# Performance work log

Measured on AMD Instinct MI355X. Metric: run time of the kernel, lower is better.

## Reference

```python
import jax, jax.numpy as jnp
import numpy as np

B, N, NS, D, H = 32, 4096, 16, 512, 8
DH = D // H          # dims_per_head = 64
DFF = 4 * D          # ff_mlp hidden
SCALE = DH ** -0.5
EPS = 1e-8           # slot-attention renorm eps
LN_EPS = 1e-5        # torch LayerNorm default
ITERS = 3


def layer_norm(x, g, b):
    mu = jnp.mean(x, axis=-1, keepdims=True)
    var = jnp.mean((x - mu) ** 2, axis=-1, keepdims=True)
    return (x - mu) * jax.lax.rsqrt(var + LN_EPS) * g + b


def setup_inputs() -> dict:
    key = jax.random.key(0)
    ks = jax.random.split(key, 8)
    s = 0.02
    return {
        "inputs": jax.random.normal(ks[0], (B, N, D), jnp.float32),
        "conditioning": jax.random.normal(ks[1], (B, NS, D), jnp.float32),
        # norm_input
        "ln_in_g": jnp.ones((D,), jnp.float32),
        "ln_in_b": jnp.zeros((D,), jnp.float32),
        # projections (no bias: use_projection_bias=False)
        "Wk": jax.random.normal(ks[2], (D, D), jnp.float32) * s,
        "Wv": jax.random.normal(ks[3], (D, D), jnp.float32) * s,
        "Wq": jax.random.normal(ks[4], (D, D), jnp.float32) * s,
        "Wo": jax.random.normal(ks[5], (D, D), jnp.float32) * s,
        # norm_slots / norm_slots_ff_mlp
        "ln_s_g": jnp.ones((D,), jnp.float32),
        "ln_s_b": jnp.zeros((D,), jnp.float32),
        "ln_f_g": jnp.ones((D,), jnp.float32),
        "ln_f_b": jnp.zeros((D,), jnp.float32),
        # ff_mlp: Linear(D,4D) -> ReLU -> Linear(4D,D)
        "W1": jax.random.normal(ks[6], (D, DFF), jnp.float32) * s,
        "b1": jnp.zeros((DFF,), jnp.float32),
        "W2": jax.random.normal(ks[7], (DFF, D), jnp.float32) * s,
        "b2": jnp.zeros((D,), jnp.float32),
    }


def reference(inputs, conditioning, ln_in_g, ln_in_b, Wk, Wv, Wq, Wo,
              ln_s_g, ln_s_b, ln_f_g, ln_f_b, W1, b1, W2, b2):
    b = inputs.shape[0]
    x = layer_norm(inputs, ln_in_g, ln_in_b)                 # [b, n, D]
    k = (x @ Wk.T).reshape(b, N, H, DH)                      # [b, n, h, dh]
    v = (x @ Wv.T).reshape(b, N, H, DH)

    slots = conditioning
    attn_mean = None
    for _ in range(ITERS):
        slots_prev = slots
        s = layer_norm(slots, ln_s_g, ln_s_b)
        q = (s @ Wq.T).reshape(b, NS, H, DH)                 # [b, ns, h, dh]
        dots = jnp.einsum("bihd,bjhd->bihj", q, k) * SCALE   # [b, ns, h, n]
        # softmax over flattened (slots, heads) axis, per input location j
        attn = jax.nn.softmax(dots.reshape(b, NS * H, N), axis=1)
        attn = attn.reshape(b, NS, H, N)
        attn_before = attn
        attn = attn + EPS
        attn = attn / jnp.sum(attn, axis=-1, keepdims=True)  # renorm over j
        updates = jnp.einsum("bjhd,bihj->bihd", v, attn)     # [b, ns, h, dh]
        updates = updates.reshape(b, NS, D)
        slots = updates @ Wo.T + slots_prev                  # to_o + residual
        slots_prev_ff = slots
        s2 = layer_norm(slots, ln_f_g, ln_f_b)
        s2 = jax.nn.relu(s2 @ W1 + b1) @ W2 + b2             # ff_mlp
        slots = s2 + slots_prev_ff
        attn_mean = jnp.mean(attn_before, axis=2)            # [b, ns, n]
    return slots, attn_mean
```

## Files before the change

kernel.cpp:

```cpp
#include <hip/hip_runtime.h>
#include <cstdint>
#include <cstddef>

typedef __attribute__((ext_vector_type(8))) short short8;
typedef __attribute__((ext_vector_type(4))) short short4v;
typedef __attribute__((ext_vector_type(8))) __bf16 bf16x8;
typedef __attribute__((ext_vector_type(4))) float f32x4;
typedef unsigned short u16;

static constexpr int Bb = 32, Nn = 4096, NSs = 16, Dd = 512, Hh = 8, DFF = 2048;
static constexpr float SCALE = 0.125f;
static constexpr float EPSR  = 1e-8f;
static constexpr float LN_EPS = 1e-5f;
static constexpr int JS = 16;

__device__ __forceinline__ u16 f2b(float x) {
  union { float f; uint32_t u; } a; a.f = x;
  uint32_t r = a.u + 0x7fffu + ((a.u >> 16) & 1u);
  return (u16)(r >> 16);
}
__device__ __forceinline__ float b2f(u16 x) {
  union { uint32_t u; float f; } a; a.u = ((uint32_t)x) << 16; return a.f;
}

__device__ __forceinline__ f32x4 mfma16(short8 a, short8 b, f32x4 c) {
  return __builtin_amdgcn_mfma_f32_16x16x32_bf16(
      __builtin_bit_cast(bf16x8, a), __builtin_bit_cast(bf16x8, b), c, 0, 0, 0);
}

__device__ __forceinline__ void gload16(const u16* g, u16* l) {
  __builtin_amdgcn_global_load_lds(
      (const __attribute__((address_space(1))) void*)g,
      (__attribute__((address_space(3))) void*)l, 16, 0, 0);
}

__global__ __launch_bounds__(256) void ln_rows(const float* __restrict__ src,
    const float* __restrict__ g, const float* __restrict__ bt,
    u16* __restrict__ dst, int R) {
  int row = blockIdx.x * 4 + (threadIdx.x >> 6);
  if (row >= R) return;
  int lane = threadIdx.x & 63;
  const float* p = src + (size_t)row * Dd + lane * 8;
  float4 u0 = *(const float4*)p;
  float4 u1 = *(const float4*)(p + 4);
  float x[8] = {u0.x,u0.y,u0.z,u0.w,u1.x,u1.y,u1.z,u1.w};
  float s = 0.f, s2 = 0.f;
#pragma unroll
  for (int e = 0; e < 8; ++e) { s += x[e]; s2 += x[e]*x[e]; }
#pragma unroll
  for (int m = 1; m < 64; m <<= 1) { s += __shfl_xor(s, m); s2 += __shfl_xor(s2, m); }
  float mean = s * (1.f/512.f);
  float var  = s2 * (1.f/512.f) - mean*mean;
  float rstd = rsqrtf(var + LN_EPS);
  union { u16 o[8]; short8 v; } ou;
#pragma unroll
  for (int e = 0; e < 8; ++e)
    ou.o[e] = f2b((x[e]-mean)*rstd*g[lane*8+e] + bt[lane*8+e]);
  *(short8*)(dst + (size_t)row * Dd + lane * 8) = ou.v;
}

__global__ __launch_bounds__(512, 2) void gemm_kv(const u16* __restrict__ A,
    const u16* __restrict__ Bk, const u16* __restrict__ Bv,
    u16* __restrict__ Ck, u16* __restrict__ CvT) {
  __shared__ u16 lA[2][256*64];
  __shared__ u16 lK[2][128*64];
  __shared__ u16 lV[2][128*64];
  const int tid = threadIdx.x, lane = tid & 63, wid = tid >> 6;
  const int wr = wid >> 2, wn = wid & 3;
  const int n = blockIdx.x;
  const int orig = (n & 7) * 256 + (n >> 3);
  const int bm = (orig >> 2) * 256, bn = (orig & 3) * 128;
  const size_t BN = (size_t)Bb * Nn;
  f32x4 ak[8][2] = {};
  f32x4 av[8][2] = {};
  const int sr = lane >> 3;
  const int ss = ((lane & 7) ^ (sr & 7)) * 8;
  const int li = lane & 15, lk = lane >> 4;
#define STG_A(buf, tt, h) do { \
    gload16(A + (size_t)(bm + (h)*128 + wid*16 + sr) * Dd + (tt)*64 + ss, \
            &lA[buf][((h)*128 + wid*16) * 64]); \
    gload16(A + (size_t)(bm + (h)*128 + wid*16 + 8 + sr) * Dd + (tt)*64 + ss, \
            &lA[buf][((h)*128 + wid*16 + 8) * 64]); \
  } while (0)
#define STG_K(buf, tt) do { \
    gload16(Bk + (size_t)(bn + wid*16 + sr) * Dd + (tt)*64 + ss, \
            &lK[buf][(wid*16) * 64]); \
    gload16(Bk + (size_t)(bn + wid*16 + 8 + sr) * Dd + (tt)*64 + ss, \
            &lK[buf][(wid*16 + 8) * 64]); \
  } while (0)
#define STG_V(buf, tt) do { \
    gload16(Bv + (size_t)(bn + wid*16 + sr) * Dd + (tt)*64 + ss, \
            &lV[buf][(wid*16) * 64]); \
    gload16(Bv + (size_t)(bn + wid*16 + 8 + sr) * Dd + (tt)*64 + ss, \
            &lV[buf][(wid*16 + 8) * 64]); \
  } while (0)
#define PH_ENTER() do { \
    __builtin_amdgcn_sched_barrier(0); \
    __builtin_amdgcn_s_barrier(); \
    asm volatile("s_waitcnt lgkmcnt(0)" ::: "memory"); \
    __builtin_amdgcn_sched_barrier(0); \
    __builtin_amdgcn_s_setprio(1); \
  } while (0)
#define PH_EXIT() do { \
    __builtin_amdgcn_s_setprio(0); \
    __builtin_amdgcn_sched_barrier(0); \
    __builtin_amdgcn_s_barrier(); \
    __builtin_amdgcn_sched_barrier(0); \
  } while (0)
#define PH_EXIT_VM(nvm) do { \
    __builtin_amdgcn_s_setprio(0); \
    __builtin_amdgcn_sched_barrier(0); \
    if (nvm) asm volatile("s_waitcnt vmcnt(2)" ::: "memory"); \
    else     asm volatile("s_waitcnt vmcnt(0)" ::: "memory"); \
    __builtin_amdgcn_sched_barrier(0); \
    __builtin_amdgcn_s_barrier(); \
    __builtin_amdgcn_sched_barrier(0); \
  } while (0)
  STG_A(0, 0, 0);
  STG_A(0, 0, 1);
  STG_K(0, 0);
  STG_V(0, 0);
  asm volatile("s_waitcnt vmcnt(2)" ::: "memory");
  __builtin_amdgcn_sched_barrier(0);
  __builtin_amdgcn_s_barrier();
  __builtin_amdgcn_sched_barrier(0);
  for (int t = 0; t < 8; ++t) {
    const int cb = t & 1, nb = cb ^ 1, tn = t + 1;
    const bool nl = (t != 7);
    short8 afA[4][2], afB[4][2], kf[2][2], vf[2][2];
#pragma unroll
    for (int m = 0; m < 4; ++m)
#pragma unroll
      for (int ks = 0; ks < 2; ++ks)
        afA[m][ks] = *(const short8*)&lA[cb][(wr*128 + m*16 + li)*64
                                            + (((ks*4 + lk) ^ (li & 7))*8)];
#pragma unroll
    for (int c = 0; c < 2; ++c)
#pragma unroll
      for (int ks = 0; ks < 2; ++ks)
        kf[c][ks] = *(const short8*)&lK[cb][(wn*32 + c*16 + li)*64
                                            + (((ks*4 + lk) ^ (li & 7))*8)];
    if (nl) STG_A(nb, tn, 0);
    PH_ENTER();
#pragma unroll
    for (int m = 0; m < 4; ++m)
#pragma unroll
      for (int c = 0; c < 2; ++c)
#pragma unroll
        for (int ks = 0; ks < 2; ++ks)
          ak[m][c] = mfma16(kf[c][ks], afA[m][ks], ak[m][c]);
    PH_EXIT_VM(nl);
#pragma unroll
    for (int c = 0; c < 2; ++c)
#pragma unroll
      for (int ks = 0; ks < 2; ++ks)
        vf[c][ks] = *(const short8*)&lV[cb][(wn*32 + c*16 + li)*64
                                            + (((ks*4 + lk) ^ (li & 7))*8)];
    if (nl) STG_A(nb, tn, 1);
    PH_ENTER();
#pragma unroll
    for (int m = 0; m < 4; ++m)
#pragma unroll
      for (int c = 0; c < 2; ++c)
#pragma unroll
        for (int ks = 0; ks < 2; ++ks)
          av[m][c] = mfma16(afA[m][ks], vf[c][ks], av[m][c]);
    PH_EXIT();
#pragma unroll
    for (int m = 0; m < 4; ++m)
#pragma unroll
      for (int ks = 0; ks < 2; ++ks)
        afB[m][ks] = *(const short8*)&lA[cb][(wr*128 + (m + 4)*16 + li)*64
                                            + (((ks*4 + lk) ^ (li & 7))*8)];
    if (nl) STG_K(nb, tn);
    PH_ENTER();
#pragma unroll
    for (int m = 0; m < 4; ++m)
#pragma unroll
      for (int c = 0; c < 2; ++c)
#pragma unroll
        for (int ks = 0; ks < 2; ++ks)
          ak[m + 4][c] = mfma16(kf[c][ks], afB[m][ks], ak[m + 4][c]);
    PH_EXIT();
    if (nl) STG_V(nb, tn);
    PH_ENTER();
#pragma unroll
    for (int m = 0; m < 4; ++m)
#pragma unroll
      for (int c = 0; c < 2; ++c)
#pragma unroll
        for (int ks = 0; ks < 2; ++ks)
          av[m + 4][c] = mfma16(afB[m][ks], vf[c][ks], av[m + 4][c]);
    PH_EXIT_VM(nl);
  }
#undef STG_A
#undef STG_K
#undef STG_V
#undef PH_ENTER
#undef PH_EXIT
#undef PH_EXIT_VM
#pragma unroll
  for (int m = 0; m < 8; ++m)
#pragma unroll
    for (int c = 0; c < 2; ++c) {
      {
        int row = bm + wr*128 + m*16 + li;
        int c0  = bn + wn*32 + c*16 + lk*4;
        f32x4 vk = ak[m][c];
        union { u16 o[4]; short4v v4; } ou;
#pragma unroll
        for (int r = 0; r < 4; ++r) ou.o[r] = f2b(vk[r]);
        *(short4v*)&Ck[(size_t)row * Dd + c0] = ou.v4;
      }
      {
        int col = bn + wn*32 + c*16 + li;
        int r0  = bm + wr*128 + m*16 + lk*4;
        f32x4 vv = av[m][c];
        union { u16 o[4]; short4v v4; } ou;
#pragma unroll
        for (int r = 0; r < 4; ++r) ou.o[r] = f2b(vv[r]);
        *(short4v*)&CvT[(size_t)col * BN + r0] = ou.v4;
      }
    }
}

template<int EP>
__global__ __launch_bounds__(256) void gemm64(const u16* __restrict__ A,
    const u16* __restrict__ Bw, void* __restrict__ Cp,
    const float* __restrict__ bias, const float* __restrict__ res,
    int N, int K) {
  const int lane = threadIdx.x & 63, wid = threadIdx.x >> 6;
  const int wr = wid >> 1, wc = wid & 1;
  const int bm = blockIdx.y * 64, bn = blockIdx.x * 64;
  const int li = lane & 15, lk = lane >> 4;
  f32x4 acc[2][2] = {};
  const u16* Ap = A  + (size_t)(bm + wr*32 + li) * K + lk*8;
  const u16* Bp = Bw + (size_t)(bn + wc*32 + li) * K + lk*8;
#pragma unroll 4
  for (int k0 = 0; k0 < K; k0 += 32) {
    short8 af[2], bf[2];
    af[0] = *(const short8*)(Ap + k0);
    af[1] = *(const short8*)(Ap + (size_t)16*K + k0);
    bf[0] = *(const short8*)(Bp + k0);
    bf[1] = *(const short8*)(Bp + (size_t)16*K + k0);
#pragma unroll
    for (int m = 0; m < 2; ++m)
#pragma unroll
      for (int nn2 = 0; nn2 < 2; ++nn2)
        acc[m][nn2] = mfma16(bf[nn2], af[m], acc[m][nn2]);
  }
#pragma unroll
  for (int m = 0; m < 2; ++m)
#pragma unroll
    for (int nn2 = 0; nn2 < 2; ++nn2) {
      int row = bm + wr*32 + m*16 + li;
      int c0  = bn + wc*32 + nn2*16 + lk*4;
      size_t off = (size_t)row * N + c0;
      f32x4 v = acc[m][nn2];
      if constexpr (EP == 0) {
        union { u16 o[4]; short4v v4; } ou;
#pragma unroll
        for (int r = 0; r < 4; ++r) ou.o[r] = f2b(v[r]);
        *(short4v*)&((u16*)Cp)[off] = ou.v4;
      } else if constexpr (EP == 1) {
        float4 rr = *(const float4*)&res[off];
        float4 o = {v[0] + rr.x, v[1] + rr.y, v[2] + rr.z, v[3] + rr.w};
        *(float4*)&((float*)Cp)[off] = o;
      } else if constexpr (EP == 2) {
        float4 bb = *(const float4*)&bias[c0];
        union { u16 o[4]; short4v v4; } ou;
        float x0 = v[0] + bb.x, x1 = v[1] + bb.y, x2 = v[2] + bb.z, x3 = v[3] + bb.w;
        ou.o[0] = f2b(x0 > 0.f ? x0 : 0.f); ou.o[1] = f2b(x1 > 0.f ? x1 : 0.f);
        ou.o[2] = f2b(x2 > 0.f ? x2 : 0.f); ou.o[3] = f2b(x3 > 0.f ? x3 : 0.f);
        *(short4v*)&((u16*)Cp)[off] = ou.v4;
      } else {
        float4 bb = *(const float4*)&bias[c0];
        float4 rr = *(const float4*)&res[off];
        float4 o = {v[0] + bb.x + rr.x, v[1] + bb.y + rr.y,
                    v[2] + bb.z + rr.z, v[3] + bb.w + rr.w};
        *(float4*)&((float*)Cp)[off] = o;
      }
    }
}

__global__ __launch_bounds__(512, 4) void attn_f(const u16* __restrict__ q,
    const u16* __restrict__ kk, const u16* __restrict__ vT,
    float* __restrict__ rowsum, float* __restrict__ Tpart,
    float* __restrict__ attn_mean) {
  const int js = blockIdx.x, b = blockIdx.y;
  const int tid = threadIdx.x, lane = tid & 63, h = tid >> 6;
  __shared__ float redM[8][64];
  __shared__ float redS[8][64];
  __shared__ u16 P2[8][16][72];
  const int li = lane & 15, lk = lane >> 4;
  const size_t BN = (size_t)Bb * Nn;
  const u16* qb = q + (((size_t)b*16 + li)*8 + h)*64 + lk*8;
  short8 a0 = *(const short8*)qb;
  short8 a1 = *(const short8*)(qb + 32);
  f32x4 apv[4] = {};
  float rs_acc[4] = {0.f, 0.f, 0.f, 0.f};
  for (int t2 = 0; t2 < 4; ++t2) {
    const int j0 = js * 256 + t2 * 64;
    f32x4 dt[4];
#pragma unroll
    for (int n = 0; n < 4; ++n) {
      const u16* kb = kk + ((size_t)b*Nn + j0 + n*16 + li)*Dd + h*64 + lk*8;
      f32x4 acc = {};
      acc = mfma16(a0, *(const short8*)kb, acc);
      acc = mfma16(a1, *(const short8*)(kb + 32), acc);
#pragma unroll
      for (int r = 0; r < 4; ++r) dt[n][r] = acc[r] * SCALE;
    }
#pragma unroll
    for (int n = 0; n < 4; ++n) {
      float v = fmaxf(fmaxf(dt[n][0], dt[n][1]), fmaxf(dt[n][2], dt[n][3]));
      v = fmaxf(v, __shfl_xor(v, 16));
      v = fmaxf(v, __shfl_xor(v, 32));
      if (lk == 0) redM[h][n*16 + li] = v;
    }
    __syncthreads();
    float M[4];
#pragma unroll
    for (int n = 0; n < 4; ++n) {
      float m2 = redM[0][n*16 + li];
#pragma unroll
      for (int p = 1; p < 8; ++p) m2 = fmaxf(m2, redM[p][n*16 + li]);
      M[n] = m2;
    }
#pragma unroll
    for (int n = 0; n < 4; ++n) {
      float s = 0.f;
#pragma unroll
      for (int r = 0; r < 4; ++r) { dt[n][r] = __expf(dt[n][r] - M[n]); s += dt[n][r]; }
      s += __shfl_xor(s, 16);
      s += __shfl_xor(s, 32);
      if (lk == 0) redS[h][n*16 + li] = s;
    }
    __syncthreads();
#pragma unroll
    for (int n = 0; n < 4; ++n) {
      float s2 = redS[0][n*16 + li];
#pragma unroll
      for (int p = 1; p < 8; ++p) s2 += redS[p][n*16 + li];
      float inv = 1.f / s2;
#pragma unroll
      for (int r = 0; r < 4; ++r) dt[n][r] = dt[n][r] * inv + EPSR;
    }
#pragma unroll
    for (int n = 0; n < 4; ++n)
#pragma unroll
      for (int r = 0; r < 4; ++r)
        P2[h][lk*4 + r][n*16 + li] = f2b(dt[n][r]);
#pragma unroll
    for (int r = 0; r < 4; ++r) {
      float v = dt[0][r] + dt[1][r] + dt[2][r] + dt[3][r];
      v += __shfl_xor(v, 1); v += __shfl_xor(v, 2);
      v += __shfl_xor(v, 4); v += __shfl_xor(v, 8);
      rs_acc[r] += v;
    }
    short8 pa0 = *(const short8*)&P2[h][li][lk*8];
    short8 pa1 = *(const short8*)&P2[h][li][32 + lk*8];
#pragma unroll
    for (int n = 0; n < 4; ++n) {
      const u16* vb = vT + (size_t)(h*64 + n*16 + li)*BN + (size_t)b*Nn + j0 + lk*8;
      apv[n] = mfma16(*(const short8*)vb, pa0, apv[n]);
      apv[n] = mfma16(*(const short8*)(vb + 32), pa1, apv[n]);
    }
    if (attn_mean != nullptr) {
      __syncthreads();
      int j = tid & 63;
#pragma unroll
      for (int ii = 0; ii < 2; ++ii) {
        int i = (tid >> 6) + ii*8;
        float sm = 0.f;
#pragma unroll
        for (int hh = 0; hh < 8; ++hh) sm += b2f(P2[hh][i][j]);
        attn_mean[((size_t)b*16 + i)*Nn + j0 + j] = sm * 0.125f - EPSR;
      }
      __syncthreads();
    }
  }
  float* Tout = Tpart + (((size_t)js * Bb + b) * 8 + h) * 16 * 64;
#pragma unroll
  for (int n = 0; n < 4; ++n) {
    float4 o = {apv[n][0], apv[n][1], apv[n][2], apv[n][3]};
    *(float4*)&Tout[(size_t)li * 64 + n*16 + lk*4] = o;
  }
  if (li == 0)
#pragma unroll
    for (int r = 0; r < 4; ++r)
      atomicAdd(&rowsum[b*128 + (lk*4 + r)*8 + h], rs_acc[r]);
}

__global__ void upd_c(const float* __restrict__ Tpart,
    const float* __restrict__ rs, u16* __restrict__ updb) {
  int idx = blockIdx.x * 256 + threadIdx.x;
  int o = idx & 511, bi = idx >> 9;
  int b = bi >> 4, i = bi & 15;
  int h = o >> 6, d = o & 63;
  size_t base = (((size_t)b * 8 + h) * 16 + i) * 64 + d;
  const size_t stride = (size_t)Bb * 8 * 16 * 64;
  float t = 0.f;
#pragma unroll
  for (int p = 0; p < JS; ++p) t += Tpart[base + p * stride];
  updb[idx] = f2b(t / rs[b * 128 + i * 8 + h]);
}

__global__ void cvt_w(const float* __restrict__ s, u16* __restrict__ d, int n) {
  int i = blockIdx.x*256 + threadIdx.x;
  if (i < n) d[i] = f2b(s[i]);
}
__global__ __launch_bounds__(256) void tr_cvt(const float* __restrict__ s,
    u16* __restrict__ d, int R, int C) {
  __shared__ u16 t[32][33];
  const int c0 = blockIdx.x*32, r0 = blockIdx.y*32;
  const int tr = threadIdx.x >> 3, tc4 = (threadIdx.x & 7)*4;
  float4 v = *(const float4*)&s[(size_t)(r0+tr)*C + c0 + tc4];
  t[tr][tc4+0] = f2b(v.x); t[tr][tc4+1] = f2b(v.y);
  t[tr][tc4+2] = f2b(v.z); t[tr][tc4+3] = f2b(v.w);
  __syncthreads();
  const int oc = threadIdx.x >> 3, or4 = (threadIdx.x & 7)*4;
  union { u16 o[4]; short4v v4; } ou;
#pragma unroll
  for (int e = 0; e < 4; ++e) ou.o[e] = t[or4+e][oc];
  *(short4v*)&d[(size_t)(c0+oc)*R + r0 + or4] = ou.v4;
}
__global__ void copy_f32v4(const float* __restrict__ s, float* __restrict__ d, int n4) {
  int i = blockIdx.x*256 + threadIdx.x;
  if (i < n4) ((float4*)d)[i] = ((const float4*)s)[i];
}

extern "C" void kernel_launch(void* const* d_in, const int* in_sizes, int n_in,
                              void* d_out, int out_size, void* d_ws, size_t ws_size,
                              hipStream_t stream) {
  (void)in_sizes; (void)n_in; (void)out_size; (void)ws_size;
  const float* inputs  = (const float*)d_in[0];
  const float* cond    = (const float*)d_in[1];
  const float* ln_in_g = (const float*)d_in[2];
  const float* ln_in_b = (const float*)d_in[3];
  const float* Wk = (const float*)d_in[4];
  const float* Wv = (const float*)d_in[5];
  const float* Wq = (const float*)d_in[6];
  const float* Wo = (const float*)d_in[7];
  const float* ln_s_g = (const float*)d_in[8];
  const float* ln_s_b = (const float*)d_in[9];
  const float* ln_f_g = (const float*)d_in[10];
  const float* ln_f_b = (const float*)d_in[11];
  const float* W1 = (const float*)d_in[12];
  const float* b1 = (const float*)d_in[13];
  const float* W2 = (const float*)d_in[14];
  const float* b2 = (const float*)d_in[15];
  float* out_slots = (float*)d_out;
  float* out_amean = (float*)d_out + (size_t)Bb*NSs*Dd;

  char* w = (char*)d_ws;
  auto alloc = [&](size_t bytes) {
    char* p = w; w += (bytes + 255) & ~(size_t)255; return p;
  };
  u16*  xn    = (u16*)alloc((size_t)Bb*Nn*Dd*2);
  u16*  kbuf  = (u16*)alloc((size_t)Bb*Nn*Dd*2);
  u16*  vT    = (u16*)alloc((size_t)Bb*Nn*Dd*2);
  float* Tpart = (float*)alloc((size_t)JS*Bb*8*16*64*4);
  float* slots = (float*)alloc((size_t)Bb*NSs*Dd*4);
  u16*  qb    = (u16*)alloc((size_t)Bb*NSs*Dd*2);
  u16*  snb   = (u16*)alloc((size_t)Bb*NSs*Dd*2);
  u16*  s2nb  = (u16*)alloc((size_t)Bb*NSs*Dd*2);
  u16*  h1b   = (u16*)alloc((size_t)Bb*NSs*DFF*2);
  u16*  updb  = (u16*)alloc((size_t)Bb*NSs*Dd*2);
  float* rowsum = (float*)alloc((size_t)Bb*128*3*4);
  u16*  wkb = (u16*)alloc(262144*2);
  u16*  wvb = (u16*)alloc(262144*2);
  u16*  wqb = (u16*)alloc(262144*2);
  u16*  wob = (u16*)alloc(262144*2);
  u16*  w1t = (u16*)alloc((size_t)1048576*2);
  u16*  w2t = (u16*)alloc((size_t)1048576*2);

  cvt_w<<<1024, 256, 0, stream>>>(Wk, wkb, 262144);
  cvt_w<<<1024, 256, 0, stream>>>(Wv, wvb, 262144);
  cvt_w<<<1024, 256, 0, stream>>>(Wq, wqb, 262144);
  cvt_w<<<1024, 256, 0, stream>>>(Wo, wob, 262144);
  tr_cvt<<<dim3(64, 16), 256, 0, stream>>>(W1, w1t, 512, 2048);
  tr_cvt<<<dim3(16, 64), 256, 0, stream>>>(W2, w2t, 2048, 512);
  copy_f32v4<<<256, 256, 0, stream>>>(cond, slots, 65536);
  (void)hipMemsetAsync(rowsum, 0, (size_t)Bb*128*3*4, stream);
  ln_rows<<<Bb*Nn/4, 256, 0, stream>>>(inputs, ln_in_g, ln_in_b, xn, Bb*Nn);
  gemm_kv<<<2048, 512, 0, stream>>>(xn, wkb, wvb, kbuf, vT);

  for (int it = 0; it < 3; ++it) {
    float* rsp = rowsum + (size_t)it * Bb * 128;
    ln_rows<<<128, 256, 0, stream>>>(slots, ln_s_g, ln_s_b, snb, Bb*NSs);
    gemm64<0><<<dim3(8, 8), 256, 0, stream>>>(snb, wqb, qb, nullptr, nullptr, 512, 512);
    attn_f<<<dim3(JS, Bb), 512, 0, stream>>>(qb, kbuf, vT, rsp, Tpart,
                                             it == 2 ? out_amean : nullptr);
    upd_c<<<1024, 256, 0, stream>>>(Tpart, rsp, updb);
    gemm64<1><<<dim3(8, 8), 256, 0, stream>>>(updb, wob, slots, nullptr, slots, 512, 512);
    ln_rows<<<128, 256, 0, stream>>>(slots, ln_f_g, ln_f_b, s2nb, Bb*NSs);
    gemm64<2><<<dim3(32, 8), 256, 0, stream>>>(s2nb, w1t, h1b, b1, nullptr, 2048, 512);
    gemm64<3><<<dim3(8, 8), 256, 0, stream>>>(h1b, w2t, slots, b2, slots, 512, 2048);
  }
  copy_f32v4<<<256, 256, 0, stream>>>(slots, out_slots, 65536);
}
```

Before: 700.3 us.

## Fuse slot LayerNorms and partial-sum combine into the small GEMM prologues

```diff
diff --git a/kernel.cpp b/kernel.cpp
--- a/kernel.cpp
+++ b/kernel.cpp
@@ -225,8 +225,135 @@
 }
 
 template<int EP>
-__global__ __launch_bounds__(256) void gemm64(const u16* __restrict__ A,
+__device__ __forceinline__ void gemm_from_lds(const u16* lAbase,
     const u16* __restrict__ Bw, void* __restrict__ Cp,
+    const float* __restrict__ bias, const float* __restrict__ res,
+    int bm, int bn, int N) {
+  const int lane = threadIdx.x & 63, wid = threadIdx.x >> 6;
+  const int wr = wid >> 1, wc = wid & 1;
+  const int li = lane & 15, lk = lane >> 4;
+  f32x4 acc[2][2] = {};
+  const u16* Bp = Bw + (size_t)(bn + wc*32 + li) * Dd + lk*8;
+#pragma unroll 4
+  for (int k0 = 0; k0 < Dd; k0 += 32) {
+    short8 af[2], bf[2];
+#pragma unroll
+    for (int m = 0; m < 2; ++m) {
+      int row = wr*32 + m*16 + li;
+      af[m] = *(const short8*)&lAbase[row*512 + (((k0 >> 3) + lk) ^ (row & 7))*8];
+    }
+    bf[0] = *(const short8*)(Bp + k0);
+    bf[1] = *(const short8*)(Bp + (size_t)16*Dd + k0);
+#pragma unroll
+    for (int m = 0; m < 2; ++m)
+#pragma unroll
+      for (int nn2 = 0; nn2 < 2; ++nn2)
+        acc[m][nn2] = mfma16(bf[nn2], af[m], acc[m][nn2]);
+  }
+#pragma unroll
+  for (int m = 0; m < 2; ++m)
+#pragma unroll
+    for (int nn2 = 0; nn2 < 2; ++nn2) {
+      int row = bm + wr*32 + m*16 + li;
+      int c0  = bn + wc*32 + nn2*16 + lk*4;
+      size_t off = (size_t)row * N + c0;
+      f32x4 v = acc[m][nn2];
+      if constexpr (EP == 0) {
+        union { u16 o[4]; short4v v4; } ou;
+#pragma unroll
+        for (int r = 0; r < 4; ++r) ou.o[r] = f2b(v[r]);
+        *(short4v*)&((u16*)Cp)[off] = ou.v4;
+      } else if constexpr (EP == 1) {
+        float4 rr = *(const float4*)&res[off];
+        float4 o = {v[0] + rr.x, v[1] + rr.y, v[2] + rr.z, v[3] + rr.w};
+        *(float4*)&((float*)Cp)[off] = o;
+      } else if constexpr (EP == 2) {
+        float4 bb = *(const float4*)&bias[c0];
+        union { u16 o[4]; short4v v4; } ou;
+        float x0 = v[0] + bb.x, x1 = v[1] + bb.y, x2 = v[2] + bb.z, x3 = v[3] + bb.w;
+        ou.o[0] = f2b(x0 > 0.f ? x0 : 0.f); ou.o[1] = f2b(x1 > 0.f ? x1 : 0.f);
+        ou.o[2] = f2b(x2 > 0.f ? x2 : 0.f); ou.o[3] = f2b(x3 > 0.f ? x3 : 0.f);
+        *(short4v*)&((u16*)Cp)[off] = ou.v4;
+      }
+    }
+}
+
+template<int EP>
+__global__ __launch_bounds__(256) void lngemm(const float* __restrict__ src,
+    const float* __restrict__ g, const float* __restrict__ bt,
+    const u16* __restrict__ Bw, void* __restrict__ Cp,
+    const float* __restrict__ bias, int N) {
+  __shared__ u16 lA[64 * 512];
+  const int tid = threadIdx.x;
+  const int bm = blockIdx.y * 64, bn = blockIdx.x * 64;
+  {
+    const int r = tid >> 2, q4 = tid & 3;
+    const float* p = src + (size_t)(bm + r) * Dd + q4 * 128;
+    float s = 0.f, s2 = 0.f;
+#pragma unroll
+    for (int c4 = 0; c4 < 32; ++c4) {
+      float4 v = *(const float4*)(p + c4 * 4);
+      s += v.x + v.y + v.z + v.w;
+      s2 += v.x*v.x + v.y*v.y + v.z*v.z + v.w*v.w;
+    }
+    s += __shfl_xor(s, 1); s2 += __shfl_xor(s2, 1);
+    s += __shfl_xor(s, 2); s2 += __shfl_xor(s2, 2);
+    float mean = s * (1.f/512.f);
+    float var  = s2 * (1.f/512.f) - mean*mean;
+    float rstd = rsqrtf(var + LN_EPS);
+#pragma unroll
+    for (int e = 0; e < 16; ++e) {
+      int k = q4 * 128 + e * 8;
+      union { u16 o[8]; short8 v; } ou;
+#pragma unroll
+      for (int j = 0; j < 8; ++j)
+        ou.o[j] = f2b((p[e*8 + j - 0] - mean) * rstd * g[k + j] + bt[k + j]);
+      int slot = (k >> 3) ^ (r & 7);
+      *(short8*)&lA[r * 512 + slot * 8] = ou.v;
+    }
+  }
+  __syncthreads();
+  gemm_from_lds<EP>(lA, Bw, Cp, bias, nullptr, bm, bn, N);
+}
+
+__global__ __launch_bounds__(256) void cmbgemm(const float* __restrict__ Tpart,
+    const float* __restrict__ rs, const u16* __restrict__ Bw,
+    float* __restrict__ Cp, const float* __restrict__ res) {
+  __shared__ u16 lA[64 * 512];
+  const int tid = threadIdx.x;
+  const int bm = blockIdx.y * 64, bn = blockIdx.x * 64;
+  {
+    const int r = tid >> 2, q4 = tid & 3;
+    const int bi = bm + r, b = bi >> 4, i = bi & 15;
+    const size_t stride = (size_t)Bb * 8 * 16 * 64;
+#pragma unroll
+    for (int e = 0; e < 16; ++e) {
+      int c = q4 * 128 + e * 8;
+      int h = c >> 6, d = c & 63;
+      size_t base = (((size_t)b * 8 + h) * 16 + i) * 64 + d;
+      float4 a0 = {0.f,0.f,0.f,0.f}, a1 = {0.f,0.f,0.f,0.f};
+      for (int p = 0; p < JS; ++p) {
+        float4 v0 = *(const float4*)&Tpart[base + p * stride];
+        float4 v1 = *(const float4*)&Tpart[base + p * stride + 4];
+        a0.x += v0.x; a0.y += v0.y; a0.z += v0.z; a0.w += v0.w;
+        a1.x += v1.x; a1.y += v1.y; a1.z += v1.z; a1.w += v1.w;
+      }
+      float inv = 1.f / rs[b * 128 + i * 8 + h];
+      union { u16 o[8]; short8 v; } ou;
+      ou.o[0] = f2b(a0.x*inv); ou.o[1] = f2b(a0.y*inv);
+      ou.o[2] = f2b(a0.z*inv); ou.o[3] = f2b(a0.w*inv);
+      ou.o[4] = f2b(a1.x*inv); ou.o[5] = f2b(a1.y*inv);
+      ou.o[6] = f2b(a1.z*inv); ou.o[7] = f2b(a1.w*inv);
+      int slot = (c >> 3) ^ (r & 7);
+      *(short8*)&lA[r * 512 + slot * 8] = ou.v;
+    }
+  }
+  __syncthreads();
+  gemm_from_lds<1>(lA, Bw, Cp, nullptr, res, bm, bn, 512);
+}
+
+__global__ __launch_bounds__(256) void gemm64_ep3(const u16* __restrict__ A,
+    const u16* __restrict__ Bw, float* __restrict__ Cp,
     const float* __restrict__ bias, const float* __restrict__ res,
     int N, int K) {
   const int lane = threadIdx.x & 63, wid = threadIdx.x >> 6;
@@ -257,29 +384,11 @@
       int c0  = bn + wc*32 + nn2*16 + lk*4;
       size_t off = (size_t)row * N + c0;
       f32x4 v = acc[m][nn2];
-      if constexpr (EP == 0) {
-        union { u16 o[4]; short4v v4; } ou;
-#pragma unroll
-        for (int r = 0; r < 4; ++r) ou.o[r] = f2b(v[r]);
-        *(short4v*)&((u16*)Cp)[off] = ou.v4;
-      } else if constexpr (EP == 1) {
-        float4 rr = *(const float4*)&res[off];
-        float4 o = {v[0] + rr.x, v[1] + rr.y, v[2] + rr.z, v[3] + rr.w};
-        *(float4*)&((float*)Cp)[off] = o;
-      } else if constexpr (EP == 2) {
-        float4 bb = *(const float4*)&bias[c0];
-        union { u16 o[4]; short4v v4; } ou;
-        float x0 = v[0] + bb.x, x1 = v[1] + bb.y, x2 = v[2] + bb.z, x3 = v[3] + bb.w;
-        ou.o[0] = f2b(x0 > 0.f ? x0 : 0.f); ou.o[1] = f2b(x1 > 0.f ? x1 : 0.f);
-        ou.o[2] = f2b(x2 > 0.f ? x2 : 0.f); ou.o[3] = f2b(x3 > 0.f ? x3 : 0.f);
-        *(short4v*)&((u16*)Cp)[off] = ou.v4;
-      } else {
-        float4 bb = *(const float4*)&bias[c0];
-        float4 rr = *(const float4*)&res[off];
-        float4 o = {v[0] + bb.x + rr.x, v[1] + bb.y + rr.y,
-                    v[2] + bb.z + rr.z, v[3] + bb.w + rr.w};
-        *(float4*)&((float*)Cp)[off] = o;
-      }
+      float4 bb = *(const float4*)&bias[c0];
+      float4 rr = *(const float4*)&res[off];
+      float4 o = {v[0] + bb.x + rr.x, v[1] + bb.y + rr.y,
+                  v[2] + bb.z + rr.z, v[3] + bb.w + rr.w};
+      *(float4*)&Cp[off] = o;
     }
 }
 
@@ -390,20 +499,6 @@
 #pragma unroll
     for (int r = 0; r < 4; ++r)
       atomicAdd(&rowsum[b*128 + (lk*4 + r)*8 + h], rs_acc[r]);
-}
-
-__global__ void upd_c(const float* __restrict__ Tpart,
-    const float* __restrict__ rs, u16* __restrict__ updb) {
-  int idx = blockIdx.x * 256 + threadIdx.x;
-  int o = idx & 511, bi = idx >> 9;
-  int b = bi >> 4, i = bi & 15;
-  int h = o >> 6, d = o & 63;
-  size_t base = (((size_t)b * 8 + h) * 16 + i) * 64 + d;
-  const size_t stride = (size_t)Bb * 8 * 16 * 64;
-  float t = 0.f;
-#pragma unroll
-  for (int p = 0; p < JS; ++p) t += Tpart[base + p * stride];
-  updb[idx] = f2b(t / rs[b * 128 + i * 8 + h]);
 }
 
 __global__ void cvt_w(const float* __restrict__ s, u16* __restrict__ d, int n) {
@@ -463,10 +558,7 @@
   float* Tpart = (float*)alloc((size_t)JS*Bb*8*16*64*4);
   float* slots = (float*)alloc((size_t)Bb*NSs*Dd*4);
   u16*  qb    = (u16*)alloc((size_t)Bb*NSs*Dd*2);
-  u16*  snb   = (u16*)alloc((size_t)Bb*NSs*Dd*2);
-  u16*  s2nb  = (u16*)alloc((size_t)Bb*NSs*Dd*2);
   u16*  h1b   = (u16*)alloc((size_t)Bb*NSs*DFF*2);
-  u16*  updb  = (u16*)alloc((size_t)Bb*NSs*Dd*2);
   float* rowsum = (float*)alloc((size_t)Bb*128*3*4);
   u16*  wkb = (u16*)alloc(262144*2);
   u16*  wvb = (u16*)alloc(262144*2);
@@ -488,15 +580,15 @@
 
   for (int it = 0; it < 3; ++it) {
     float* rsp = rowsum + (size_t)it * Bb * 128;
-    ln_rows<<<128, 256, 0, stream>>>(slots, ln_s_g, ln_s_b, snb, Bb*NSs);
-    gemm64<0><<<dim3(8, 8), 256, 0, stream>>>(snb, wqb, qb, nullptr, nullptr, 512, 512);
+    lngemm<0><<<dim3(8, 8), 256, 0, stream>>>(slots, ln_s_g, ln_s_b, wqb, qb,
+                                              nullptr, 512);
     attn_f<<<dim3(JS, Bb), 512, 0, stream>>>(qb, kbuf, vT, rsp, Tpart,
                                              it == 2 ? out_amean : nullptr);
-    upd_c<<<1024, 256, 0, stream>>>(Tpart, rsp, updb);
-    gemm64<1><<<dim3(8, 8), 256, 0, stream>>>(updb, wob, slots, nullptr, slots, 512, 512);
-    ln_rows<<<128, 256, 0, stream>>>(slots, ln_f_g, ln_f_b, s2nb, Bb*NSs);
-    gemm64<2><<<dim3(32, 8), 256, 0, stream>>>(s2nb, w1t, h1b, b1, nullptr, 2048, 512);
-    gemm64<3><<<dim3(8, 8), 256, 0, stream>>>(h1b, w2t, slots, b2, slots, 512, 2048);
+    cmbgemm<<<dim3(8, 8), 256, 0, stream>>>(Tpart, rsp, wob, slots, slots);
+    lngemm<2><<<dim3(32, 8), 256, 0, stream>>>(slots, ln_f_g, ln_f_b, w1t, h1b,
+                                               b1, 2048);
+    gemm64_ep3<<<dim3(8, 8), 256, 0, stream>>>(h1b, w2t, slots, b2, slots,
+                                               512, 2048);
   }
   copy_f32v4<<<256, 256, 0, stream>>>(slots, out_slots, 65536);
 }
```

New measurement: 1.007 ms. 43.7% more time.

## Fuse slot LayerNorm and Q projection into attention kernel

Applied to the files above, without the earlier changes.

```diff
diff --git a/kernel.cpp b/kernel.cpp
--- a/kernel.cpp
+++ b/kernel.cpp
@@ -257,12 +257,7 @@
       int c0  = bn + wc*32 + nn2*16 + lk*4;
       size_t off = (size_t)row * N + c0;
       f32x4 v = acc[m][nn2];
-      if constexpr (EP == 0) {
-        union { u16 o[4]; short4v v4; } ou;
-#pragma unroll
-        for (int r = 0; r < 4; ++r) ou.o[r] = f2b(v[r]);
-        *(short4v*)&((u16*)Cp)[off] = ou.v4;
-      } else if constexpr (EP == 1) {
+      if constexpr (EP == 1) {
         float4 rr = *(const float4*)&res[off];
         float4 o = {v[0] + rr.x, v[1] + rr.y, v[2] + rr.z, v[3] + rr.w};
         *(float4*)&((float*)Cp)[off] = o;
@@ -283,20 +278,69 @@
     }
 }
 
-__global__ __launch_bounds__(512, 4) void attn_f(const u16* __restrict__ q,
-    const u16* __restrict__ kk, const u16* __restrict__ vT,
-    float* __restrict__ rowsum, float* __restrict__ Tpart,
-    float* __restrict__ attn_mean) {
+__global__ __launch_bounds__(512, 4) void attn_f(const float* __restrict__ slots,
+    const float* __restrict__ lng, const float* __restrict__ lnb,
+    const u16* __restrict__ Wq, const u16* __restrict__ kk,
+    const u16* __restrict__ vT, float* __restrict__ rowsum,
+    float* __restrict__ Tpart, float* __restrict__ attn_mean) {
   const int js = blockIdx.x, b = blockIdx.y;
   const int tid = threadIdx.x, lane = tid & 63, h = tid >> 6;
   __shared__ float redM[8][64];
   __shared__ float redS[8][64];
   __shared__ u16 P2[8][16][72];
+  __shared__ u16 ls[16 * 520];
+  __shared__ u16 lq[16 * 520];
   const int li = lane & 15, lk = lane >> 4;
   const size_t BN = (size_t)Bb * Nn;
-  const u16* qb = q + (((size_t)b*16 + li)*8 + h)*64 + lk*8;
-  short8 a0 = *(const short8*)qb;
-  short8 a1 = *(const short8*)(qb + 32);
+  {
+    const int r = 2*h + (lane >> 5);
+    const int c0 = (lane & 31) * 16;
+    const float* p = slots + ((size_t)b*16 + r) * Dd + c0;
+    float4 v0 = *(const float4*)p;
+    float4 v1 = *(const float4*)(p + 4);
+    float4 v2 = *(const float4*)(p + 8);
+    float4 v3 = *(const float4*)(p + 12);
+    float x[16] = {v0.x,v0.y,v0.z,v0.w, v1.x,v1.y,v1.z,v1.w,
+                   v2.x,v2.y,v2.z,v2.w, v3.x,v3.y,v3.z,v3.w};
+    float s = 0.f, s2 = 0.f;
+#pragma unroll
+    for (int e = 0; e < 16; ++e) { s += x[e]; s2 += x[e]*x[e]; }
+#pragma unroll
+    for (int m = 1; m < 32; m <<= 1) { s += __shfl_xor(s, m); s2 += __shfl_xor(s2, m); }
+    float mean = s * (1.f/512.f);
+    float var  = s2 * (1.f/512.f) - mean*mean;
+    float rstd = rsqrtf(var + LN_EPS);
+    union { u16 o[8]; short8 v; } oa, ob;
+#pragma unroll
+    for (int e = 0; e < 8; ++e) {
+      oa.o[e] = f2b((x[e]   - mean) * rstd * lng[c0 + e]     + lnb[c0 + e]);
+      ob.o[e] = f2b((x[e+8] - mean) * rstd * lng[c0 + 8 + e] + lnb[c0 + 8 + e]);
+    }
+    *(short8*)&ls[r * 520 + c0] = oa.v;
+    *(short8*)&ls[r * 520 + c0 + 8] = ob.v;
+  }
+  __syncthreads();
+  {
+    f32x4 qacc[4] = {};
+    const u16* Wp = Wq + (size_t)(h*64 + li) * Dd + lk*8;
+#pragma unroll 4
+    for (int k0 = 0; k0 < 512; k0 += 32) {
+      short8 af = *(const short8*)&ls[li*520 + k0 + lk*8];
+#pragma unroll
+      for (int n = 0; n < 4; ++n) {
+        short8 bf = *(const short8*)(Wp + (size_t)(n*16)*Dd + k0);
+        qacc[n] = mfma16(af, bf, qacc[n]);
+      }
+    }
+#pragma unroll
+    for (int n = 0; n < 4; ++n)
+#pragma unroll
+      for (int r = 0; r < 4; ++r)
+        lq[(lk*4 + r)*520 + h*64 + n*16 + li] = f2b(qacc[n][r]);
+  }
+  __syncthreads();
+  short8 a0 = *(const short8*)&lq[li*520 + h*64 + lk*8];
+  short8 a1 = *(const short8*)&lq[li*520 + h*64 + 32 + lk*8];
   f32x4 apv[4] = {};
   float rs_acc[4] = {0.f, 0.f, 0.f, 0.f};
   for (int t2 = 0; t2 < 4; ++t2) {
@@ -462,8 +506,6 @@
   u16*  vT    = (u16*)alloc((size_t)Bb*Nn*Dd*2);
   float* Tpart = (float*)alloc((size_t)JS*Bb*8*16*64*4);
   float* slots = (float*)alloc((size_t)Bb*NSs*Dd*4);
-  u16*  qb    = (u16*)alloc((size_t)Bb*NSs*Dd*2);
-  u16*  snb   = (u16*)alloc((size_t)Bb*NSs*Dd*2);
   u16*  s2nb  = (u16*)alloc((size_t)Bb*NSs*Dd*2);
   u16*  h1b   = (u16*)alloc((size_t)Bb*NSs*DFF*2);
   u16*  updb  = (u16*)alloc((size_t)Bb*NSs*Dd*2);
@@ -488,9 +530,8 @@
 
   for (int it = 0; it < 3; ++it) {
     float* rsp = rowsum + (size_t)it * Bb * 128;
-    ln_rows<<<128, 256, 0, stream>>>(slots, ln_s_g, ln_s_b, snb, Bb*NSs);
-    gemm64<0><<<dim3(8, 8), 256, 0, stream>>>(snb, wqb, qb, nullptr, nullptr, 512, 512);
-    attn_f<<<dim3(JS, Bb), 512, 0, stream>>>(qb, kbuf, vT, rsp, Tpart,
+    attn_f<<<dim3(JS, Bb), 512, 0, stream>>>(slots, ln_s_g, ln_s_b, wqb,
+                                             kbuf, vT, rsp, Tpart,
                                              it == 2 ? out_amean : nullptr);
     upd_c<<<1024, 256, 0, stream>>>(Tpart, rsp, updb);
     gemm64<1><<<dim3(8, 8), 256, 0, stream>>>(updb, wob, slots, nullptr, slots, 512, 512);
```

New measurement: 756.3 us. +8.0%, slower.
